# Optimization experiments

Hardware: AMD Instinct MI355X
Metric: run time of the kernel (lower is better)

The kernel has to match this reference:

```python
import jax, jax.numpy as jnp
import numpy as np
from jax import lax


def setup_inputs() -> dict:
    key = jax.random.key(0)
    k1, k2 = jax.random.split(key)
    B, C_out, C_in, K, H, W = 16, 128, 128, 3, 64, 64
    features = jax.random.normal(k1, (B, C_in, H, W), dtype=jnp.float32)
    dynamic_kernel = jax.random.normal(k2, (B, C_out, C_in, K, K), dtype=jnp.float32)
    return {"features": features, "dynamic_kernel": dynamic_kernel}


def reference(features, dynamic_kernel):
    # Per-sample dynamic conv. unfold+bmm in torch == cross-correlation (conv2d)
    # with the per-sample kernel; we express it as a vmapped implicit-GEMM conv
    # instead of materializing the (C_in*K*K, H*W) unfold buffer.
    padding = 1

    def conv_one(x, w):  # x: (C_in, H, W), w: (C_out, C_in, K, K)
        return lax.conv_general_dilated(
            x[None],                      # (1, C_in, H, W)
            w,
            window_strides=(1, 1),
            padding=[(padding, padding), (padding, padding)],
            dimension_numbers=("NCHW", "OIHW", "NCHW"),
        )[0]                              # (C_out, H, W)

    return jax.vmap(conv_one)(features, dynamic_kernel)  # (B, C_out, H, W)
```

## Files before the change

kernel.cpp:

```cpp
#include <hip/hip_runtime.h>
#include <stdint.h>

#define BATCH 16
#define CIN   128
#define COUT  128
#define IMG_H 64
#define IMG_W 64
#define HW    4096
#define KTOT  1152
#define XH    66
#define XW    66
#define NCQ   16
#define NSTEPS 18
#define ASTEP 8192

typedef __attribute__((ext_vector_type(8))) __bf16 bf16x8;
typedef __attribute__((ext_vector_type(4))) float  f32x4;
typedef __attribute__((address_space(1))) const void* gas_p;
typedef __attribute__((address_space(3))) void*       las_p;

static __device__ __forceinline__ unsigned short f2bf(float f) {
  union { float f; uint32_t u; } c; c.f = f;
  uint32_t r = c.u + 0x7fffu + ((c.u >> 16) & 1u);
  return (unsigned short)(r >> 16);
}

static __device__ __forceinline__ bf16x8 ldg8(const unsigned short* p) {
  uint4 w = *(const uint4*)p;
  return __builtin_bit_cast(bf16x8, w);
}

static __device__ __forceinline__ void gload_lds16(const unsigned short* g, unsigned short* l) {
  __builtin_amdgcn_global_load_lds((gas_p)g, (las_p)l, 16, 0, 0);
}

__global__ void prep_fused(const float* __restrict__ x, const float* __restrict__ w,
                           unsigned short* __restrict__ wt4, unsigned short* __restrict__ xpad) {
  const int t = threadIdx.x;
  if (blockIdx.x < BATCH * IMG_H) {
    __shared__ uint32_t tile[64 * 68];
    const int b = blockIdx.x & 15;
    const int h = blockIdx.x >> 4;
    const float* xb = x + (size_t)b * CIN * HW + h * IMG_W;
    uint4* xp4 = (uint4*)xpad;

    const int lane16 = t & 15;
    const int g      = t >> 4;
#pragma unroll
    for (int it = 0; it < 4; ++it) {
      const int ci = it * 32 + g * 2;
      const float4 va = *(const float4*)(xb + (size_t)ci * HW + lane16 * 4);
      const float4 vb = *(const float4*)(xb + (size_t)(ci + 1) * HW + lane16 * 4);
      const float av[4] = {va.x, va.y, va.z, va.w};
      const float bv[4] = {vb.x, vb.y, vb.z, vb.w};
#pragma unroll
      for (int cc = 0; cc < 4; ++cc)
        tile[(lane16 * 4 + cc) * 68 + it * 16 + g] =
            (uint32_t)f2bf(av[cc]) | ((uint32_t)f2bf(bv[cc]) << 16);
    }
    __syncthreads();

    const uint32_t rbase = ((uint32_t)b * XH + h + 1) * NCQ;
#pragma unroll
    for (int it = 0; it < 4; ++it) {
      const int o   = it * 256 + t;
      const int cqg = o >> 6;
      const int wc  = o & 63;
      const uint4 v = *(const uint4*)&tile[wc * 68 + cqg * 4];
      xp4[(rbase + cqg) * XW + wc + 1] = v;
    }
    if (t < 32) {
      const int cqg = t & 15;
      const int col = (t >> 4) ? 65 : 0;
      xp4[(rbase + cqg) * XW + col] = make_uint4(0, 0, 0, 0);
    }
    if (h == 0) {
      const uint32_t r0  = (uint32_t)b * XH * NCQ * XW;
      const uint32_t r65 = ((uint32_t)b * XH + 65) * NCQ * XW;
      for (int i = t; i < NCQ * XW; i += 256) {
        xp4[r0 + i]  = make_uint4(0, 0, 0, 0);
        xp4[r65 + i] = make_uint4(0, 0, 0, 0);
      }
    }
  } else {
    const int idx  = blockIdx.x - BATCH * IMG_H;
    const int b    = idx & 15;
    const int step = idx >> 4;
    const int khkw = step >> 1;
    const int cib  = (step & 1) << 6;
    const float* wb = w + (size_t)b * COUT * KTOT;
    unsigned short* dst = wt4 + ((size_t)b * NSTEPS + step) * ASTEP;
#pragma unroll
    for (int i = 0; i < 4; ++i) {
      const int c  = i * 256 + t;
      const int cq = c >> 7;
      const int co = c & 127;
      const int ci0 = cib + cq * 8;
      const float* src = wb + (size_t)co * KTOT + (size_t)ci0 * 9 + khkw;
      uint32_t p[4];
#pragma unroll
      for (int e = 0; e < 4; ++e)
        p[e] = (uint32_t)f2bf(src[(2 * e) * 9]) | ((uint32_t)f2bf(src[(2 * e + 1) * 9]) << 16);
      *(uint4*)&dst[(size_t)c * 8] = make_uint4(p[0], p[1], p[2], p[3]);
    }
  }
}

__global__ __launch_bounds__(256, 2) void dynconv_gemm(
    const unsigned short* __restrict__ wt4,
    const unsigned short* __restrict__ xpad,
    float* __restrict__ out) {
  __shared__ alignas(16) unsigned short slab[4 * NCQ * 64 * 8];

  const int t    = threadIdx.x;
  const int b    = blockIdx.y;
  const int oh0  = blockIdx.x * 2;

  const int lane = t & 63;
  const int wave = t >> 6;
  const int wm   = (wave & 1) << 6;
  const int osub = wave >> 1;
  const int l15  = lane & 15;
  const int quad = lane >> 4;

  {
    const unsigned short* xsrc = xpad +
        ((((size_t)b * XH + oh0) * NCQ) * XW + 1 + lane) * 8;
#pragma unroll
    for (int p = 0; p < 16; ++p) {
      const int seg = p * 4 + wave;
      gload_lds16(xsrc + (size_t)seg * XW * 8, &slab[(p * 256 + wave * 64) * 8]);
    }
  }
  __syncthreads();

  const unsigned short* wbase = wt4 + (size_t)b * NSTEPS * ASTEP + (size_t)(quad * 128 + wm + l15) * 8;

  f32x4 acc[4][4] = {};
  bf16x8 afA[8], afB[8];

#define LOADA(S, AF)                                                          \
  {                                                                           \
    const unsigned short* wstep_ = wbase + (size_t)(S) * ASTEP;               \
    _Pragma("unroll") for (int ks_ = 0; ks_ < 2; ++ks_)                       \
      _Pragma("unroll") for (int i_ = 0; i_ < 4; ++i_)                        \
        AF[ks_ * 4 + i_] = ldg8(wstep_ + (ks_ * 512 + i_ * 16) * 8);          \
  }

#define COMPUTE(S, AF)                                                        \
  {                                                                           \
    const int khkw_ = (S) >> 1;                                               \
    const int kh_ = khkw_ / 3, kw_ = khkw_ % 3;                               \
    _Pragma("unroll") for (int ks_ = 0; ks_ < 2; ++ks_) {                     \
      const int cq_ = ((S) & 1) * 8 + ks_ * 4 + quad;                         \
      const int rb_ = ((osub + kh_) * NCQ + cq_) * 64;                        \
      bf16x8 bf[4];                                                           \
      _Pragma("unroll") for (int j_ = 0; j_ < 4; ++j_) {                      \
        int cm_ = j_ * 16 + l15 + kw_ - 1;                                    \
        if (j_ == 0) cm_ = cm_ < 0 ? 0 : cm_;                                 \
        if (j_ == 3) cm_ = cm_ > 63 ? 63 : cm_;                               \
        bf[j_] = *(const bf16x8*)&slab[(rb_ + cm_) * 8];                      \
      }                                                                       \
      if (kw_ == 0 && l15 == 0)  bf[0] = (bf16x8){};                          \
      if (kw_ == 2 && l15 == 15) bf[3] = (bf16x8){};                          \
      _Pragma("unroll") for (int i_ = 0; i_ < 4; ++i_)                        \
        _Pragma("unroll") for (int j_ = 0; j_ < 4; ++j_)                      \
          acc[i_][j_] = __builtin_amdgcn_mfma_f32_16x16x32_bf16(              \
              AF[ks_ * 4 + i_], bf[j_], acc[i_][j_], 0, 0, 0);                \
    }                                                                         \
  }

  LOADA(0, afA);
#pragma unroll
  for (int s = 0; s < NSTEPS; s += 2) {
    LOADA(s + 1, afB);
    COMPUTE(s, afA);
    if (s + 2 < NSTEPS) LOADA(s + 2, afA);
    COMPUTE(s + 1, afB);
  }
#undef LOADA
#undef COMPUTE

  float* obase = out + (size_t)b * COUT * HW + (oh0 + osub) * 64;
#pragma unroll
  for (int i = 0; i < 4; ++i) {
#pragma unroll
    for (int r = 0; r < 4; ++r) {
      float* orow = obase + (size_t)(wm + i * 16 + quad * 4 + r) * HW;
#pragma unroll
      for (int j = 0; j < 4; ++j)
        orow[j * 16 + l15] = acc[i][j][r];
    }
  }
}

__global__ void dynconv_naive(const float* __restrict__ x, const float* __restrict__ w,
                              float* __restrict__ out) {
  const int o   = blockIdx.x * 256 + threadIdx.x;
  const int pix = o & (HW - 1);
  const int co  = (o >> 12) & (COUT - 1);
  const int b   = o >> 19;
  const int oh  = pix >> 6, ow = pix & 63;
  const float* xb = x + (size_t)b * CIN * HW;
  const float* wb = w + ((size_t)b * COUT + co) * CIN * 9;
  float s = 0.f;
  for (int ci = 0; ci < CIN; ++ci) {
    const float* xc = xb + ci * HW;
    const float* wc = wb + ci * 9;
#pragma unroll
    for (int kh = 0; kh < 3; ++kh) {
      const int ih = oh + kh - 1;
      if ((unsigned)ih >= IMG_H) continue;
#pragma unroll
      for (int kw = 0; kw < 3; ++kw) {
        const int iw = ow + kw - 1;
        if ((unsigned)iw >= IMG_W) continue;
        s += xc[ih * IMG_W + iw] * wc[kh * 3 + kw];
      }
    }
  }
  out[o] = s;
}

extern "C" void kernel_launch(void* const* d_in, const int* in_sizes, int n_in,
                              void* d_out, int out_size, void* d_ws, size_t ws_size,
                              hipStream_t stream) {
  const float* x = (const float*)d_in[0];
  const float* w = (const float*)d_in[1];
  float* out = (float*)d_out;

  const size_t wt_bytes = (size_t)BATCH * NSTEPS * ASTEP * sizeof(unsigned short);
  const size_t xp_bytes = (size_t)BATCH * XH * NCQ * XW * 8 * sizeof(unsigned short);

  if (ws_size >= wt_bytes + xp_bytes) {
    unsigned short* wt4  = (unsigned short*)d_ws;
    unsigned short* xpad = (unsigned short*)((char*)d_ws + wt_bytes);
    prep_fused<<<BATCH * IMG_H + BATCH * NSTEPS, 256, 0, stream>>>(x, w, wt4, xpad);
    dim3 grid(IMG_H / 2, BATCH);
    dynconv_gemm<<<grid, 256, 0, stream>>>(wt4, xpad, out);
  } else {
    dynconv_naive<<<(BATCH * COUT * HW) / 256, 256, 0, stream>>>(x, w, out);
  }
}
```

Measured before the change: 131.9 us.

## Stage weight tiles into double-buffered LDS via async global-to-LDS loads

Weight (A) fragments are no longer loaded by each wave straight from global memory into registers. They are now copied into a double-buffered LDS tile with global_load_lds, once per block per half-step, and read from LDS. The loop is split into 36 smaller K steps with a block barrier at the end of each. This removes duplicated global reads of A across waves that share rows, at the cost of extra LDS capacity, a barrier every step, and a less unrolled loop.

```diff
diff --git a/kernel.cpp b/kernel.cpp
--- a/kernel.cpp
+++ b/kernel.cpp
@@ -11,8 +11,8 @@
 #define XH    66
 #define XW    66
 #define NCQ   16
-#define NSTEPS 18
-#define ASTEP 8192
+#define NST32 36
+#define ATILE 4096
 
 typedef __attribute__((ext_vector_type(8))) __bf16 bf16x8;
 typedef __attribute__((ext_vector_type(4))) float  f32x4;
@@ -23,11 +23,6 @@
   union { float f; uint32_t u; } c; c.f = f;
   uint32_t r = c.u + 0x7fffu + ((c.u >> 16) & 1u);
   return (unsigned short)(r >> 16);
-}
-
-static __device__ __forceinline__ bf16x8 ldg8(const unsigned short* p) {
-  uint4 w = *(const uint4*)p;
-  return __builtin_bit_cast(bf16x8, w);
 }
 
 static __device__ __forceinline__ void gload_lds16(const unsigned short* g, unsigned short* l) {
@@ -89,7 +84,7 @@
     const int khkw = step >> 1;
     const int cib  = (step & 1) << 6;
     const float* wb = w + (size_t)b * COUT * KTOT;
-    unsigned short* dst = wt4 + ((size_t)b * NSTEPS + step) * ASTEP;
+    unsigned short* dst = wt4 + ((size_t)b * 18 + step) * 8192;
 #pragma unroll
     for (int i = 0; i < 4; ++i) {
       const int c  = i * 256 + t;
@@ -111,6 +106,7 @@
     const unsigned short* __restrict__ xpad,
     float* __restrict__ out) {
   __shared__ alignas(16) unsigned short slab[4 * NCQ * 64 * 8];
+  __shared__ alignas(16) unsigned short Abuf[2][ATILE];
 
   const int t    = threadIdx.x;
   const int b    = blockIdx.y;
@@ -132,54 +128,53 @@
       gload_lds16(xsrc + (size_t)seg * XW * 8, &slab[(p * 256 + wave * 64) * 8]);
     }
   }
+
+  const unsigned short* wbase = wt4 + (size_t)b * NST32 * ATILE + (size_t)t * 8;
+
+#define STAGEA(S, BUF)                                                        \
+  {                                                                           \
+    const unsigned short* src_ = wbase + (size_t)(S) * ATILE;                 \
+    gload_lds16(src_,        &Abuf[BUF][(wave * 64) * 8]);                    \
+    gload_lds16(src_ + 2048, &Abuf[BUF][(256 + wave * 64) * 8]);              \
+  }
+
+  STAGEA(0, 0);
   __syncthreads();
 
-  const unsigned short* wbase = wt4 + (size_t)b * NSTEPS * ASTEP + (size_t)(quad * 128 + wm + l15) * 8;
-
   f32x4 acc[4][4] = {};
-  bf16x8 afA[8], afB[8];
-
-#define LOADA(S, AF)                                                          \
-  {                                                                           \
-    const unsigned short* wstep_ = wbase + (size_t)(S) * ASTEP;               \
-    _Pragma("unroll") for (int ks_ = 0; ks_ < 2; ++ks_)                       \
-      _Pragma("unroll") for (int i_ = 0; i_ < 4; ++i_)                        \
-        AF[ks_ * 4 + i_] = ldg8(wstep_ + (ks_ * 512 + i_ * 16) * 8);          \
-  }
-
-#define COMPUTE(S, AF)                                                        \
-  {                                                                           \
-    const int khkw_ = (S) >> 1;                                               \
-    const int kh_ = khkw_ / 3, kw_ = khkw_ % 3;                               \
-    _Pragma("unroll") for (int ks_ = 0; ks_ < 2; ++ks_) {                     \
-      const int cq_ = ((S) & 1) * 8 + ks_ * 4 + quad;                         \
-      const int rb_ = ((osub + kh_) * NCQ + cq_) * 64;                        \
-      bf16x8 bf[4];                                                           \
-      _Pragma("unroll") for (int j_ = 0; j_ < 4; ++j_) {                      \
-        int cm_ = j_ * 16 + l15 + kw_ - 1;                                    \
-        if (j_ == 0) cm_ = cm_ < 0 ? 0 : cm_;                                 \
-        if (j_ == 3) cm_ = cm_ > 63 ? 63 : cm_;                               \
-        bf[j_] = *(const bf16x8*)&slab[(rb_ + cm_) * 8];                      \
-      }                                                                       \
-      if (kw_ == 0 && l15 == 0)  bf[0] = (bf16x8){};                          \
-      if (kw_ == 2 && l15 == 15) bf[3] = (bf16x8){};                          \
-      _Pragma("unroll") for (int i_ = 0; i_ < 4; ++i_)                        \
-        _Pragma("unroll") for (int j_ = 0; j_ < 4; ++j_)                      \
-          acc[i_][j_] = __builtin_amdgcn_mfma_f32_16x16x32_bf16(              \
-              AF[ks_ * 4 + i_], bf[j_], acc[i_][j_], 0, 0, 0);                \
-    }                                                                         \
-  }
-
-  LOADA(0, afA);
-#pragma unroll
-  for (int s = 0; s < NSTEPS; s += 2) {
-    LOADA(s + 1, afB);
-    COMPUTE(s, afA);
-    if (s + 2 < NSTEPS) LOADA(s + 2, afA);
-    COMPUTE(s + 1, afB);
-  }
-#undef LOADA
-#undef COMPUTE
+
+  for (int s = 0; s < NST32; ++s) {
+    if (s + 1 < NST32) STAGEA(s + 1, (s + 1) & 1);
+
+    const int khkw = s >> 2;
+    const int kh   = (khkw * 11) >> 5;
+    const int kw   = khkw - kh * 3;
+    const int cq_g = ((s & 3) << 2) + quad;
+    const int rb   = ((osub + kh) * NCQ + cq_g) * 64;
+    const unsigned short* ab = &Abuf[s & 1][(quad * 128 + wm + l15) * 8];
+
+    bf16x8 af[4], bf[4];
+#pragma unroll
+    for (int i = 0; i < 4; ++i) af[i] = *(const bf16x8*)(ab + i * 16 * 8);
+#pragma unroll
+    for (int j = 0; j < 4; ++j) {
+      int cm = j * 16 + l15 + kw - 1;
+      if (j == 0) cm = cm < 0 ? 0 : cm;
+      if (j == 3) cm = cm > 63 ? 63 : cm;
+      bf[j] = *(const bf16x8*)&slab[(rb + cm) * 8];
+    }
+    if (kw == 0 && l15 == 0)  bf[0] = (bf16x8){};
+    if (kw == 2 && l15 == 15) bf[3] = (bf16x8){};
+
+#pragma unroll
+    for (int i = 0; i < 4; ++i)
+#pragma unroll
+      for (int j = 0; j < 4; ++j)
+        acc[i][j] = __builtin_amdgcn_mfma_f32_16x16x32_bf16(af[i], bf[j], acc[i][j], 0, 0, 0);
+
+    __syncthreads();
+  }
+#undef STAGEA
 
   float* obase = out + (size_t)b * COUT * HW + (oh0 + osub) * 64;
 #pragma unroll
@@ -229,13 +224,13 @@
   const float* w = (const float*)d_in[1];
   float* out = (float*)d_out;
 
-  const size_t wt_bytes = (size_t)BATCH * NSTEPS * ASTEP * sizeof(unsigned short);
+  const size_t wt_bytes = (size_t)BATCH * NST32 * ATILE * sizeof(unsigned short);
   const size_t xp_bytes = (size_t)BATCH * XH * NCQ * XW * 8 * sizeof(unsigned short);
 
   if (ws_size >= wt_bytes + xp_bytes) {
     unsigned short* wt4  = (unsigned short*)d_ws;
     unsigned short* xpad = (unsigned short*)((char*)d_ws + wt_bytes);
-    prep_fused<<<BATCH * IMG_H + BATCH * NSTEPS, 256, 0, stream>>>(x, w, wt4, xpad);
+    prep_fused<<<BATCH * IMG_H + BATCH * 18, 256, 0, stream>>>(x, w, wt4, xpad);
     dim3 grid(IMG_H / 2, BATCH);
     dynconv_gemm<<<grid, 256, 0, stream>>>(wt4, xpad, out);
   } else {
```

After: 128.0 us. -2.9%, faster.
